# Kernel optimization log

Hardware: AMD Instinct MI355X
Metric: run time of the kernel (lower is better)

## Reference

```python
import jax, jax.numpy as jnp
import numpy as np

H = 28; W = 28; N = H * W
P = N              # padded max persistence pairs per homology dimension
T = 32             # landscape resolution
K1, K2 = 2, 3      # K_max for the two topo layers
M0_1, M0_2 = 0.05, 0.2
LIMS = ((1.0, 28.0), (1.0, 28.0))


def _make_nbrs(h, w, conn8):
    idx = np.arange(h * w).reshape(h, w)
    offs = [(-1, 0), (1, 0), (0, -1), (0, 1)]
    if conn8:
        offs += [(-1, -1), (-1, 1), (1, -1), (1, 1)]
    nbrs = []
    for i in range(h):
        for j in range(w):
            cur = [idx[i + a, j + b] for a, b in offs if 0 <= i + a < h and 0 <= j + b < w]
            nbrs.append(np.asarray(cur, np.int64))
    return nbrs

_NBR4 = _make_nbrs(H, W, False)
_NBR8 = _make_nbrs(H, W, True)


def _h0_pairs(vals, nbrs):
    # 0-dim persistence pairs of a vertex-valued sublevel filtration (union-find, elder rule)
    order = np.argsort(vals, kind="stable")
    pos = np.empty(N, np.int64); pos[order] = np.arange(N)
    parent = np.arange(N); birth = np.arange(N)
    added = np.zeros(N, bool)
    bi = np.zeros(P, np.int32); di = np.zeros(P, np.int32)
    k = 0
    def find(x):
        r = x
        while parent[r] != r: r = parent[r]
        while parent[x] != r: parent[x], x = r, parent[x]
        return r
    for v in order:
        added[v] = True
        for u in nbrs[v]:
            if not added[u]: continue
            ru, rv = find(u), find(v)
            if ru == rv: continue
            if pos[birth[ru]] <= pos[birth[rv]]:
                lb = birth[rv]; parent[rv] = ru
            else:
                lb = birth[ru]; parent[ru] = rv
            if k < P:
                bi[k] = lb; di[k] = v; k += 1
    return bi, di


def _pers_pairs_np(x):
    # x: [M, N] -> (birth_idx, death_idx) each [M, 2, P]; padded pairs point at idx 0 (zero persistence)
    x = np.asarray(x, np.float64)
    M = x.shape[0]
    bi = np.zeros((M, 2, P), np.int32); di = np.zeros((M, 2, P), np.int32)
    for m in range(M):
        b0, d0 = _h0_pairs(x[m], _NBR4)      # H0: sublevel, 4-connectivity
        b1, d1 = _h0_pairs(-x[m], _NBR8)     # H1 by Alexander duality: H0 of superlevel, 8-connectivity
        bi[m, 0], di[m, 0] = b0, d0
        bi[m, 1], di[m, 1] = d1, b1          # H1 birth = vals[d1], death = vals[b1]
    return bi, di


def _grid_d2():
    xs = np.linspace(LIMS[0][0], LIMS[0][1], H)
    ys = np.linspace(LIMS[1][0], LIMS[1][1], W)
    gx, gy = np.meshgrid(xs, ys, indexing="ij")
    pts = np.stack([gx.ravel(), gy.ravel()], 1)              # [N, 2] grid coordinates
    d2 = ((pts[:, None, :] - pts[None, :, :]) ** 2).sum(-1)  # [N, N] squared distances
    si = np.argsort(d2, axis=1, kind="stable")
    return jnp.asarray(si), jnp.asarray(np.take_along_axis(d2, si, 1), jnp.float32)

_SORT_IDX, _D2S = _grid_d2()


def dtm(x_flat, m0):
    # weighted distance-to-measure on the pixel grid, r=2; x_flat: [M, N] positive weights
    bound = m0 * jnp.sum(x_flat, -1, keepdims=True)                        # [M, 1]
    ws = x_flat[:, _SORT_IDX]                                              # [M, N, N] weights in distance order
    cum = jnp.cumsum(ws, -1)
    eff = jnp.minimum(jnp.maximum(bound[..., None] - (cum - ws), 0.0), ws) # effective mass per neighbor
    return jnp.sqrt(jnp.sum(eff * _D2S, -1) / bound)                       # [M, N]


def _landscape(vals, bi, di, start, end, K):
    # persistence landscape lambda_k sampled on T points from (birth, death) critical-vertex indices
    M = vals.shape[0]
    mi = jnp.arange(M)[:, None, None]
    b = vals[mi, bi]; d = vals[mi, di]                                     # [M, 2, P]
    t = jnp.linspace(start, end, T, dtype=vals.dtype)                      # [T]
    tent = jnp.maximum(jnp.minimum(t - b[..., None], d[..., None] - t), 0.0)  # [M, 2, P, T]
    lam, _ = jax.lax.top_k(jnp.swapaxes(tent, -1, -2), K)                  # [M, 2, T, K]
    return jnp.swapaxes(lam, -1, -2).reshape(M, 2 * K * T)                 # [M, dims*K*T]


def pl_features(vals, start, end, K):
    M = vals.shape[0]
    bi, di = jax.pure_callback(
        _pers_pairs_np,
        (jax.ShapeDtypeStruct((M, 2, P), np.int32),
         jax.ShapeDtypeStruct((M, 2, P), np.int32)),
        jax.lax.stop_gradient(vals))
    return _landscape(vals, bi, di, start, end, K)


def setup_inputs():
    key = jax.random.key(0)
    ks = jax.random.split(key, 7)
    B = 64
    return {
        "input": jax.random.uniform(ks[0], (B, 1, H, W), jnp.float32, 1e-3, 1.0),
        "w_g1": 0.1 * jax.random.normal(ks[1], (32, 2 * K1 * T), jnp.float32),
        "b_g1": 0.1 * jax.random.normal(ks[2], (32,), jnp.float32),
        "w_g2": 0.1 * jax.random.normal(ks[3], (32, 2 * K2 * T), jnp.float32),
        "b_g2": 0.1 * jax.random.normal(ks[4], (32,), jnp.float32),
        "w_fc": 0.1 * jax.random.normal(ks[5], (10, 64), jnp.float32),
        "b_fc": 0.1 * jax.random.normal(ks[6], (10,), jnp.float32),
    }


def reference(input, w_g1, b_g1, w_g2, b_g2, w_fc, b_fc):
    x_flat = input.reshape(-1, N)                                        # num_channels = 1
    f1 = dtm(x_flat, M0_1)
    f2 = dtm(x_flat, M0_2)
    x1 = jax.nn.relu(pl_features(f1, 0.0, 7.0, K1) @ w_g1.T + b_g1)      # topo layer 1 (start=0, end=7, K=2)
    x2 = jax.nn.relu(pl_features(f2, 1.0, 8.0, K2) @ w_g2.T + b_g2)      # topo layer 2 (start=1, end=8, K=3)
    return jnp.concatenate([x1, x2], -1) @ w_fc.T + b_fc                 # [B, num_classes]
```

## Files before the change

kernel.cpp:

```cpp
#include <hip/hip_runtime.h>

#define HW 28
#define NPIX 784
#define NIMG 64
#define MAXD2 1459
#define MAXREC 5504

#define DXPK 41048u
#define DYPK 34949u

__global__ void consts_sums_kernel(unsigned int* __restrict__ TPK,
                                   const float* __restrict__ x,
                                   float* __restrict__ sums,
                                   float* __restrict__ xT) {
    int tid = threadIdx.x;
    if (blockIdx.x >= NPIX) {
        int m = blockIdx.x - NPIX;
        const float* xr = x + m * NPIX;
        float acc = 0.f;
        for (int j = tid; j < NPIX; j += 256) {
            float v = xr[j];
            xT[j * NIMG + m] = v;
            acc += v;
        }
        for (int off = 32; off > 0; off >>= 1) acc += __shfl_down(acc, off, 64);
        __shared__ float red[4];
        int lane = tid & 63, w = tid >> 6;
        if (lane == 0) red[w] = acc;
        __syncthreads();
        if (tid == 0) sums[m] = red[0] + red[1] + red[2] + red[3];
        return;
    }
    __shared__ int cnt[MAXD2];
    __shared__ int d2v[NPIX];
    __shared__ int wtot[4];
    int i = blockIdx.x;
    for (int b = tid; b < MAXD2; b += 256) cnt[b] = 0;
    __syncthreads();
    int ii = i / HW, ij = i % HW;
    for (int j = tid; j < NPIX; j += 256) {
        int di = ii - j / HW, dj = ij - j % HW;
        int d = di * di + dj * dj;
        d2v[j] = d;
        atomicAdd(&cnt[d], 1);
    }
    __syncthreads();
    int b0 = tid * 6;
    int lc[6];
    int s0 = 0;
    #pragma unroll
    for (int t = 0; t < 6; ++t) {
        int b = b0 + t;
        lc[t] = (b < MAXD2) ? cnt[b] : 0;
        s0 += lc[t];
    }
    int lane = tid & 63, wv = tid >> 6;
    int v = s0;
    for (int off = 1; off < 64; off <<= 1) {
        int t2 = __shfl_up(v, off, 64);
        if (lane >= off) v += t2;
    }
    if (lane == 63) wtot[wv] = v;
    __syncthreads();
    int wadd = 0;
    for (int w2 = 0; w2 < wv; ++w2) wadd += wtot[w2];
    int run = wadd + v - s0;
    __syncthreads();
    #pragma unroll
    for (int t = 0; t < 6; ++t) {
        int b = b0 + t;
        if (b < MAXD2) { cnt[b] = run; run += lc[t]; }
    }
    __syncthreads();
    for (int j = tid; j < NPIX; j += 256) {
        int d = d2v[j];
        int slot = atomicAdd(&cnt[d], 1);
        TPK[i * NPIX + slot] = (unsigned)j | ((unsigned)d << 16);
    }
}

__global__ void __launch_bounds__(64) dtm_kernel(const unsigned int* __restrict__ TPK,
                                                 const float* __restrict__ xT,
                                                 const float* __restrict__ sums,
                                                 float* __restrict__ F) {
    int lane = threadIdx.x;
    int i = blockIdx.x;
    float s = sums[lane];
    float bound1 = 0.05f * s, bound2 = 0.2f * s;
    const unsigned int* tp = TPK + (size_t)i * NPIX;
    float cum = 0.f, acc1 = 0.f, acc2 = 0.f;
    for (int t0 = 0; t0 < NPIX; t0 += 8) {
        unsigned int e[8];
        #pragma unroll
        for (int u = 0; u < 8; ++u) e[u] = tp[t0 + u];
        float w[8];
        #pragma unroll
        for (int u = 0; u < 8; ++u) w[u] = xT[(e[u] & 0xffffu) * NIMG + lane];
        #pragma unroll
        for (int u = 0; u < 8; ++u) {
            float d2 = (float)(e[u] >> 16);
            float ce = cum;
            cum += w[u];
            acc1 += fminf(fmaxf(bound1 - ce, 0.f), w[u]) * d2;
            acc2 += fminf(fmaxf(bound2 - ce, 0.f), w[u]) * d2;
        }
        if (__ballot(cum < bound2) == 0ull) break;
    }
    F[0 * NIMG * NPIX + lane * NPIX + i] = sqrtf(acc1 / bound1);
    F[1 * NIMG * NPIX + lane * NPIX + i] = sqrtf(acc2 / bound2);
}

template<int NN>
__device__ int uf_basin_run(const int* posA, const int* ordA,
                            int* bas, unsigned int* pb, int* comp,
                            int* recs, int* pairsI,
                            int2* mergeLDS, int* shInts, int* wtot16) {
    const int tid = threadIdx.x;
    const int lane = tid & 63, wv = tid >> 6;

    for (int s = tid; s < NPIX; s += 1024) {
        int si = s / HW, sj = s % HW;
        int bestPos = posA[s], best = s;
        #pragma unroll
        for (int o = 0; o < NN; ++o) {
            int dx = ((DXPK >> (2 * o)) & 3) - 1;
            int dy = ((DYPK >> (2 * o)) & 3) - 1;
            int ui = si + dx, uj = sj + dy;
            if ((unsigned)ui < (unsigned)HW && (unsigned)uj < (unsigned)HW) {
                int u = ui * HW + uj;
                int pu = posA[u];
                if (pu < bestPos) { bestPos = pu; best = u; }
            }
        }
        bas[s] = best;
    }
    __syncthreads();

    for (int it = 0; it < 10; ++it) {
        int changed = 0;
        for (int s = tid; s < NPIX; s += 1024) {
            int b = bas[s];
            int bb = bas[b];
            if (bb != b) { bas[s] = bb; changed = 1; }
        }
        if (__syncthreads_count(changed) == 0) break;
    }

    for (int s = tid; s < NPIX; s += 1024)
        pb[s] = ((unsigned)posA[s] << 10) | (unsigned)bas[s];
    __syncthreads();

    int nrec = 0;
    {
        int r = tid;
        int cnt = 0;
        int myr[NN - 1];
        int got[NN - 1];
        #pragma unroll
        for (int t = 0; t < NN - 1; ++t) { got[t] = -1; myr[t] = 0; }
        if (r > 0 && r < NPIX) {
            int v = ordA[r];
            int vi = v / HW, vj = v % HW;
            int pivot = (int)(pb[v] & 1023u);
            #pragma unroll
            for (int o = 0; o < NN; ++o) {
                int dx = ((DXPK >> (2 * o)) & 3) - 1;
                int dy = ((DYPK >> (2 * o)) & 3) - 1;
                int ui = vi + dx, uj = vj + dy;
                if ((unsigned)ui < (unsigned)HW && (unsigned)uj < (unsigned)HW) {
                    int u = ui * HW + uj;
                    unsigned e = pb[u];
                    if ((int)(e >> 10) < r) {
                        int b = (int)(e & 1023u);
                        bool dup = (b == pivot);
                        #pragma unroll
                        for (int t = 0; t < NN - 1; ++t) dup = dup || (got[t] == b);
                        if (!dup) {
                            #pragma unroll
                            for (int t = 0; t < NN - 1; ++t)
                                if (t == cnt) { got[t] = b; myr[t] = (v << 20) | (pivot << 10) | b; }
                            cnt++;
                        }
                    }
                }
            }
        }
        int p = cnt;
        for (int off = 1; off < 64; off <<= 1) {
            int t2 = __shfl_up(p, off, 64);
            if (lane >= off) p += t2;
        }
        if (lane == 63) wtot16[wv] = p;
        __syncthreads();
        int wadd = 0;
        for (int w2 = 0; w2 < wv; ++w2) wadd += wtot16[w2];
        int tot = 0;
        #pragma unroll
        for (int w2 = 0; w2 < 16; ++w2) tot += wtot16[w2];
        int excl = wadd + p - cnt;
        #pragma unroll
        for (int t = 0; t < NN - 1; ++t)
            if (t < cnt) recs[excl + t] = myr[t];
        nrec = tot;
        __syncthreads();
    }

    int k = 0;
    for (int base = 0; base < nrec; base += 64) {
        int nrem = 0;
        if (wv == 0) {
            int idx = base + lane;
            int rec = (idx < nrec) ? recs[idx] : 0;
            int pa = (rec >> 10) & 1023, pbn = rec & 1023;
            int ka = 0, kb = 0;
            if (idx < nrec) { ka = comp[pa]; kb = comp[pbn]; }
            for (;;) {
                unsigned long long d = __ballot(ka != kb);
                if (d == 0ull) break;
                int i = (int)__ffsll((long long)d) - 1;
                int sA = __builtin_amdgcn_readlane(ka, i);
                int sB = __builtin_amdgcn_readlane(kb, i);
                int w = min(sA, sB), l = max(sA, sB);
                int sv = __builtin_amdgcn_readlane(rec, i) >> 20;
                if (lane == 0) {
                    pairsI[k] = (l & 1023) | (sv << 10);
                    mergeLDS[nrem] = make_int2(l, w);
                }
                k++;
                ka = (ka == l) ? w : ka;
                kb = (kb == l) ? w : kb;
                nrem++;
                if (nrem == 63) {
                    for (int s = lane; s < NPIX; s += 64) {
                        int cv = comp[s], c0 = cv;
                        for (int e = 0; e < nrem; ++e) {
                            int2 me = mergeLDS[e];
                            cv = (cv == me.x) ? me.y : cv;
                        }
                        if (cv != c0) comp[s] = cv;
                    }
                    if (idx < nrec) { ka = comp[pa]; kb = comp[pbn]; }
                    nrem = 0;
                }
            }
            if (lane == 0) shInts[0] = nrem;
        }
        __syncthreads();
        int nr = shInts[0];
        if (nr > 0) {
            for (int s = tid; s < NPIX; s += 1024) {
                int cv = comp[s], c0 = cv;
                for (int e = 0; e < nr; ++e) {
                    int2 me = mergeLDS[e];
                    cv = (cv == me.x) ? me.y : cv;
                }
                if (cv != c0) comp[s] = cv;
            }
        }
        __syncthreads();
    }
    if (tid == 0) shInts[1] = k;
    __syncthreads();
    return shInts[1];
}

__global__ void __launch_bounds__(1024) uf_land_kernel(const float* __restrict__ F,
                                                       float* __restrict__ LAM1,
                                                       float* __restrict__ LAM2) {
    __shared__ int posA[NPIX], ordA[NPIX], bas[NPIX], comp[NPIX], pairsI[NPIX];
    __shared__ unsigned int pbArr[NPIX];
    __shared__ alignas(16) unsigned long long key64[NPIX];
    __shared__ float fv[NPIX];
    __shared__ int recs[MAXREC];
    __shared__ int2 mergeLDS[64];
    __shared__ int shInts[2];
    __shared__ int wtot16[16];
    int tid = threadIdx.x;
    int task = blockIdx.x;
    int feat = task >> 7;
    int dir = (task >> 6) & 1;
    int m = task & 63;
    const float* fr = F + feat * NIMG * NPIX + m * NPIX;

    for (int j = tid; j < NPIX; j += 1024) {
        float f = fr[j];
        fv[j] = f;
        unsigned int b = __float_as_uint(f);
        if (dir) b = ~b;
        key64[j] = ((unsigned long long)b << 10) | (unsigned)j;
    }
    __syncthreads();

    if (tid < NPIX) {
        unsigned long long pki = key64[tid];
        int rank = 0;
        const ulonglong2* k2 = (const ulonglong2*)key64;
        for (int c = 0; c < NPIX / 2; ++c) {
            ulonglong2 kv = k2[c];
            rank += (int)(kv.x < pki) + (int)(kv.y < pki);
        }
        posA[tid] = rank;
        ordA[rank] = tid;
    }
    __syncthreads();
    for (int s = tid; s < NPIX; s += 1024) comp[s] = (posA[s] << 10) | s;

    int k;
    if (dir == 0) k = uf_basin_run<4>(posA, ordA, bas, pbArr, comp, recs, pairsI,
                                      mergeLDS, shInts, wtot16);
    else          k = uf_basin_run<8>(posA, ordA, bas, pbArr, comp, recs, pairsI,
                                      mergeLDS, shInts, wtot16);

    if (tid < 32) {
        int t = tid;
        float start = (feat == 0) ? 0.f : 1.f;
        float end   = (feat == 0) ? 7.f : 8.f;
        float tv = start + (end - start) * ((float)t / 31.f);
        float v0 = 0.f, v1 = 0.f, v2 = 0.f;
        for (int p = 0; p < k; ++p) {
            int pi = pairsI[p];
            float fb = fv[pi & 1023], fd = fv[pi >> 10];
            float bb = dir ? fd : fb;
            float dd = dir ? fb : fd;
            float tent = fmaxf(fminf(tv - bb, dd - tv), 0.f);
            if (tent > v0)      { v2 = v1; v1 = v0; v0 = tent; }
            else if (tent > v1) { v2 = v1; v1 = tent; }
            else if (tent > v2) { v2 = tent; }
        }
        if (feat == 0) {
            float* lam = LAM1 + m * 128 + dir * 64;
            lam[0 * 32 + t] = v0;
            lam[1 * 32 + t] = v1;
        } else {
            float* lam = LAM2 + m * 192 + dir * 96;
            lam[0 * 32 + t] = v0;
            lam[1 * 32 + t] = v1;
            lam[2 * 32 + t] = v2;
        }
    }
}

__global__ void mlp_kernel(const float* __restrict__ LAM1, const float* __restrict__ LAM2,
                           const float* __restrict__ w1, const float* __restrict__ b1,
                           const float* __restrict__ w2, const float* __restrict__ b2,
                           const float* __restrict__ wf, const float* __restrict__ bf,
                           float* __restrict__ out) {
    __shared__ float xc[64];
    int m = blockIdx.x;
    int n = threadIdx.x;
    if (n < 32) {
        float acc = b1[n];
        const float* l = LAM1 + m * 128;
        for (int c = 0; c < 128; ++c) acc += w1[n * 128 + c] * l[c];
        xc[n] = fmaxf(acc, 0.f);
    } else {
        int n2 = n - 32;
        float acc = b2[n2];
        const float* l = LAM2 + m * 192;
        for (int c = 0; c < 192; ++c) acc += w2[n2 * 192 + c] * l[c];
        xc[n] = fmaxf(acc, 0.f);
    }
    __syncthreads();
    if (n < 10) {
        float acc = bf[n];
        for (int c = 0; c < 64; ++c) acc += wf[n * 64 + c] * xc[c];
        out[m * 10 + n] = acc;
    }
}

extern "C" void kernel_launch(void* const* d_in, const int* in_sizes, int n_in,
                              void* d_out, int out_size, void* d_ws, size_t ws_size,
                              hipStream_t stream) {
    const float* x  = (const float*)d_in[0];
    const float* w1 = (const float*)d_in[1];
    const float* b1 = (const float*)d_in[2];
    const float* w2 = (const float*)d_in[3];
    const float* b2 = (const float*)d_in[4];
    const float* wf = (const float*)d_in[5];
    const float* bf = (const float*)d_in[6];
    float* out = (float*)d_out;

    char* ws = (char*)d_ws;
    size_t off = 0;
    unsigned int* TPK = (unsigned int*)(ws + off); off += (size_t)NPIX * NPIX * 4;
    float* XT   = (float*)(ws + off); off += (size_t)NPIX * NIMG * 4;
    float* SUMS = (float*)(ws + off); off += 256;
    float* F    = (float*)(ws + off); off += (size_t)2 * NIMG * NPIX * 4;
    float* LAM1 = (float*)(ws + off); off += (size_t)NIMG * 128 * 4;
    float* LAM2 = (float*)(ws + off); off += (size_t)NIMG * 192 * 4;

    consts_sums_kernel<<<NPIX + NIMG, 256, 0, stream>>>(TPK, x, SUMS, XT);
    dtm_kernel<<<NPIX, 64, 0, stream>>>(TPK, XT, SUMS, F);
    uf_land_kernel<<<256, 1024, 0, stream>>>(F, LAM1, LAM2);
    mlp_kernel<<<NIMG, 64, 0, stream>>>(LAM1, LAM2, w1, b1, w2, b2, wf, bf, out);
}
```

Measured before the change: 123.3 us.

## Register-block rank sort and parallelize landscape top-k across all threads

The rank-by-counting sort now has each of 196 threads compute ranks for four keys at once, so every key64 vector loaded from LDS is reused four times and LDS read traffic drops. The landscape step previously ran a serial loop over all pairs on only 32 threads. It now splits the pairs across 32 groups of 32 threads, each keeping a partial top-3 that is stored in the recs buffer. A second pass on 32 threads then merges those partials. This adds a barrier, a reduction step and reuse of recs as scratch, and fewer threads are active during the rank phase.

```diff
diff --git a/kernel.cpp b/kernel.cpp
--- a/kernel.cpp
+++ b/kernel.cpp
@@ -271,7 +271,7 @@
     __shared__ unsigned int pbArr[NPIX];
     __shared__ alignas(16) unsigned long long key64[NPIX];
     __shared__ float fv[NPIX];
-    __shared__ int recs[MAXREC];
+    __shared__ alignas(16) int recs[MAXREC];
     __shared__ int2 mergeLDS[64];
     __shared__ int shInts[2];
     __shared__ int wtot16[16];
@@ -291,16 +291,24 @@
     }
     __syncthreads();
 
-    if (tid < NPIX) {
-        unsigned long long pki = key64[tid];
-        int rank = 0;
+    if (tid < 196) {
+        unsigned long long pk0 = key64[tid];
+        unsigned long long pk1 = key64[tid + 196];
+        unsigned long long pk2 = key64[tid + 392];
+        unsigned long long pk3 = key64[tid + 588];
+        int r0 = 0, r1 = 0, r2 = 0, r3 = 0;
         const ulonglong2* k2 = (const ulonglong2*)key64;
         for (int c = 0; c < NPIX / 2; ++c) {
             ulonglong2 kv = k2[c];
-            rank += (int)(kv.x < pki) + (int)(kv.y < pki);
-        }
-        posA[tid] = rank;
-        ordA[rank] = tid;
+            r0 += (int)(kv.x < pk0) + (int)(kv.y < pk0);
+            r1 += (int)(kv.x < pk1) + (int)(kv.y < pk1);
+            r2 += (int)(kv.x < pk2) + (int)(kv.y < pk2);
+            r3 += (int)(kv.x < pk3) + (int)(kv.y < pk3);
+        }
+        posA[tid]       = r0; ordA[r0] = tid;
+        posA[tid + 196] = r1; ordA[r1] = tid + 196;
+        posA[tid + 392] = r2; ordA[r2] = tid + 392;
+        posA[tid + 588] = r3; ordA[r3] = tid + 588;
     }
     __syncthreads();
     for (int s = tid; s < NPIX; s += 1024) comp[s] = (posA[s] << 10) | s;
@@ -311,13 +319,14 @@
     else          k = uf_basin_run<8>(posA, ordA, bas, pbArr, comp, recs, pairsI,
                                       mergeLDS, shInts, wtot16);
 
-    if (tid < 32) {
-        int t = tid;
-        float start = (feat == 0) ? 0.f : 1.f;
-        float end   = (feat == 0) ? 7.f : 8.f;
+    float start = (feat == 0) ? 0.f : 1.f;
+    float end   = (feat == 0) ? 7.f : 8.f;
+    {
+        int sub = tid >> 5;
+        int t = tid & 31;
         float tv = start + (end - start) * ((float)t / 31.f);
         float v0 = 0.f, v1 = 0.f, v2 = 0.f;
-        for (int p = 0; p < k; ++p) {
+        for (int p = sub; p < k; p += 32) {
             int pi = pairsI[p];
             float fb = fv[pi & 1023], fd = fv[pi >> 10];
             float bb = dir ? fd : fb;
@@ -326,6 +335,25 @@
             if (tent > v0)      { v2 = v1; v1 = v0; v0 = tent; }
             else if (tent > v1) { v2 = v1; v1 = tent; }
             else if (tent > v2) { v2 = tent; }
+        }
+        float* part = (float*)recs;
+        int bse = (sub * 32 + t) * 3;
+        part[bse] = v0; part[bse + 1] = v1; part[bse + 2] = v2;
+    }
+    __syncthreads();
+    if (tid < 32) {
+        int t = tid;
+        const float* part = (const float*)recs;
+        float v0 = 0.f, v1 = 0.f, v2 = 0.f;
+        for (int s2 = 0; s2 < 32; ++s2) {
+            int bse = (s2 * 32 + t) * 3;
+            #pragma unroll
+            for (int q = 0; q < 3; ++q) {
+                float x = part[bse + q];
+                if (x > v0)      { v2 = v1; v1 = v0; v0 = x; }
+                else if (x > v1) { v2 = v1; v1 = x; }
+                else if (x > v2) { v2 = x; }
+            }
         }
         if (feat == 0) {
             float* lam = LAM1 + m * 128 + dir * 64;
```

New measurement: 130.1 us. 5.5% more time.

## Fuse distance sort with DTM accumulation via shared-memory order list

Applied to the files above, without the earlier changes.

The per-pixel distance counting sort now keeps its sorted neighbour list in shared memory and runs the DTM accumulation in the same block, instead of writing a 784x784 global table that a separate kernel reads back. The transpose-and-sum work moves into its own small kernel launched first. This removes about 2.4 MB of global traffic and one dependency step. In exchange, only one wave of each 256-thread block does the DTM loop, so three waves sit idle during that phase.

```diff
diff --git a/kernel.cpp b/kernel.cpp
--- a/kernel.cpp
+++ b/kernel.cpp
@@ -9,32 +9,37 @@
 #define DXPK 41048u
 #define DYPK 34949u
 
-__global__ void consts_sums_kernel(unsigned int* __restrict__ TPK,
-                                   const float* __restrict__ x,
-                                   float* __restrict__ sums,
-                                   float* __restrict__ xT) {
+__global__ void xt_sums_kernel(const float* __restrict__ x,
+                               float* __restrict__ sums,
+                               float* __restrict__ xT) {
     int tid = threadIdx.x;
-    if (blockIdx.x >= NPIX) {
-        int m = blockIdx.x - NPIX;
-        const float* xr = x + m * NPIX;
-        float acc = 0.f;
-        for (int j = tid; j < NPIX; j += 256) {
-            float v = xr[j];
-            xT[j * NIMG + m] = v;
-            acc += v;
-        }
-        for (int off = 32; off > 0; off >>= 1) acc += __shfl_down(acc, off, 64);
-        __shared__ float red[4];
-        int lane = tid & 63, w = tid >> 6;
-        if (lane == 0) red[w] = acc;
-        __syncthreads();
-        if (tid == 0) sums[m] = red[0] + red[1] + red[2] + red[3];
-        return;
-    }
+    int m = blockIdx.x;
+    const float* xr = x + m * NPIX;
+    float acc = 0.f;
+    for (int j = tid; j < NPIX; j += 256) {
+        float v = xr[j];
+        xT[j * NIMG + m] = v;
+        acc += v;
+    }
+    for (int off = 32; off > 0; off >>= 1) acc += __shfl_down(acc, off, 64);
+    __shared__ float red[4];
+    int lane = tid & 63, w = tid >> 6;
+    if (lane == 0) red[w] = acc;
+    __syncthreads();
+    if (tid == 0) sums[m] = red[0] + red[1] + red[2] + red[3];
+}
+
+__global__ void sortdtm_kernel(const float* __restrict__ x,
+                               const float* __restrict__ xT,
+                               const float* __restrict__ sums,
+                               float* __restrict__ F) {
     __shared__ int cnt[MAXD2];
     __shared__ int d2v[NPIX];
+    __shared__ unsigned int tpl[NPIX];
     __shared__ int wtot[4];
+    int tid = threadIdx.x;
     int i = blockIdx.x;
+
     for (int b = tid; b < MAXD2; b += 256) cnt[b] = 0;
     __syncthreads();
     int ii = i / HW, ij = i % HW;
@@ -75,39 +80,34 @@
     for (int j = tid; j < NPIX; j += 256) {
         int d = d2v[j];
         int slot = atomicAdd(&cnt[d], 1);
-        TPK[i * NPIX + slot] = (unsigned)j | ((unsigned)d << 16);
-    }
-}
-
-__global__ void __launch_bounds__(64) dtm_kernel(const unsigned int* __restrict__ TPK,
-                                                 const float* __restrict__ xT,
-                                                 const float* __restrict__ sums,
-                                                 float* __restrict__ F) {
-    int lane = threadIdx.x;
-    int i = blockIdx.x;
-    float s = sums[lane];
-    float bound1 = 0.05f * s, bound2 = 0.2f * s;
-    const unsigned int* tp = TPK + (size_t)i * NPIX;
-    float cum = 0.f, acc1 = 0.f, acc2 = 0.f;
-    for (int t0 = 0; t0 < NPIX; t0 += 8) {
-        unsigned int e[8];
-        #pragma unroll
-        for (int u = 0; u < 8; ++u) e[u] = tp[t0 + u];
-        float w[8];
-        #pragma unroll
-        for (int u = 0; u < 8; ++u) w[u] = xT[(e[u] & 0xffffu) * NIMG + lane];
-        #pragma unroll
-        for (int u = 0; u < 8; ++u) {
-            float d2 = (float)(e[u] >> 16);
-            float ce = cum;
-            cum += w[u];
-            acc1 += fminf(fmaxf(bound1 - ce, 0.f), w[u]) * d2;
-            acc2 += fminf(fmaxf(bound2 - ce, 0.f), w[u]) * d2;
-        }
-        if (__ballot(cum < bound2) == 0ull) break;
-    }
-    F[0 * NIMG * NPIX + lane * NPIX + i] = sqrtf(acc1 / bound1);
-    F[1 * NIMG * NPIX + lane * NPIX + i] = sqrtf(acc2 / bound2);
+        tpl[slot] = (unsigned)j | ((unsigned)d << 16);
+    }
+    __syncthreads();
+
+    if (tid < 64) {
+        float s = sums[tid];
+        float bound1 = 0.05f * s, bound2 = 0.2f * s;
+        float cum = 0.f, acc1 = 0.f, acc2 = 0.f;
+        for (int t0 = 0; t0 < NPIX; t0 += 8) {
+            unsigned int e[8];
+            #pragma unroll
+            for (int u = 0; u < 8; ++u) e[u] = tpl[t0 + u];
+            float w[8];
+            #pragma unroll
+            for (int u = 0; u < 8; ++u) w[u] = xT[(e[u] & 0xffffu) * NIMG + tid];
+            #pragma unroll
+            for (int u = 0; u < 8; ++u) {
+                float d2 = (float)(e[u] >> 16);
+                float ce = cum;
+                cum += w[u];
+                acc1 += fminf(fmaxf(bound1 - ce, 0.f), w[u]) * d2;
+                acc2 += fminf(fmaxf(bound2 - ce, 0.f), w[u]) * d2;
+            }
+            if (__ballot(cum < bound2) == 0ull) break;
+        }
+        F[0 * NIMG * NPIX + tid * NPIX + i] = sqrtf(acc1 / bound1);
+        F[1 * NIMG * NPIX + tid * NPIX + i] = sqrtf(acc2 / bound2);
+    }
 }
 
 template<int NN>
@@ -382,15 +382,14 @@
 
     char* ws = (char*)d_ws;
     size_t off = 0;
-    unsigned int* TPK = (unsigned int*)(ws + off); off += (size_t)NPIX * NPIX * 4;
     float* XT   = (float*)(ws + off); off += (size_t)NPIX * NIMG * 4;
     float* SUMS = (float*)(ws + off); off += 256;
     float* F    = (float*)(ws + off); off += (size_t)2 * NIMG * NPIX * 4;
     float* LAM1 = (float*)(ws + off); off += (size_t)NIMG * 128 * 4;
     float* LAM2 = (float*)(ws + off); off += (size_t)NIMG * 192 * 4;
 
-    consts_sums_kernel<<<NPIX + NIMG, 256, 0, stream>>>(TPK, x, SUMS, XT);
-    dtm_kernel<<<NPIX, 64, 0, stream>>>(TPK, XT, SUMS, F);
+    xt_sums_kernel<<<NIMG, 256, 0, stream>>>(x, SUMS, XT);
+    sortdtm_kernel<<<NPIX, 256, 0, stream>>>(x, XT, SUMS, F);
     uf_land_kernel<<<256, 1024, 0, stream>>>(F, LAM1, LAM2);
     mlp_kernel<<<NIMG, 64, 0, stream>>>(LAM1, LAM2, w1, b1, w2, b2, wf, bf, out);
 }
```

Result: faster. 120.5 us (-2.2%).
